# Kernel optimization log

Hardware: AMD Instinct MI355X
Metric: run time of the kernel (lower is better)

## Reference

```python
import jax, jax.numpy as jnp
import numpy as np

B, S, D, H = 4, 2048, 512, 8  # batch, seq, input_dim=feature_dim, n_heads


def setup_inputs() -> dict:
    key = jax.random.key(0)
    ks = jax.random.split(key, 12)
    s = 1.0 / np.sqrt(D)
    return {
        "q": jax.random.normal(ks[0], (B, S, D), jnp.float32),
        "k": jax.random.normal(ks[1], (B, S, D), jnp.float32),
        "v": jax.random.normal(ks[2], (B, S, D), jnp.float32),
        "mask": jax.random.randint(ks[3], (B, S), 0, 2, jnp.int32),
        "wq": jax.random.uniform(ks[4], (D, D), jnp.float32, -s, s),
        "bq": jax.random.uniform(ks[5], (D,), jnp.float32, -s, s),
        "wk": jax.random.uniform(ks[6], (D, D), jnp.float32, -s, s),
        "bk": jax.random.uniform(ks[7], (D,), jnp.float32, -s, s),
        "wv": jax.random.uniform(ks[8], (D, D), jnp.float32, -s, s),
        "bv": jax.random.uniform(ks[9], (D,), jnp.float32, -s, s),
        "wd": jax.random.uniform(ks[10], (D, D), jnp.float32, -s, s),
        "bd": jax.random.uniform(ks[11], (D,), jnp.float32, -s, s),
    }


def reference(q, k, v, mask, wq, bq, wk, bk, wv, bv, wd, bd):
    hd = D // H
    # linear projections [B,S,D]
    qp = q @ wq + bq
    kp = k @ wk + bk
    vp = v @ wv + bv
    # split heads -> [B,H,S,hd]
    split = lambda x: x.reshape(B, S, H, hd).transpose(0, 2, 1, 3)
    qh, kh, vh = split(qp), split(kp), split(vp)
    # scaled dot-product attention with additive mask [B,1,1,S]
    scores = jnp.einsum("bhqd,bhkd->bhqk", qh, kh) / np.sqrt(hd)
    scores = scores + mask.astype(scores.dtype)[:, None, None, :] * (-1e9)
    weights = jax.nn.softmax(scores, axis=-1)
    attn = jnp.einsum("bhqk,bhkd->bhqd", weights, vh)
    # merge heads -> [B,S,D], final dense
    attn = attn.transpose(0, 2, 1, 3).reshape(B, S, D)
    return attn @ wd + bd
```

## Files before the change

### kernel.cpp

```cpp
#include <hip/hip_runtime.h>
#include <hip/hip_bf16.h>
#include <cmath>

typedef __bf16 bf16;
typedef __attribute__((ext_vector_type(8))) __bf16 bf16x8;
typedef __attribute__((ext_vector_type(4))) __bf16 bf16x4;
typedef __attribute__((ext_vector_type(4))) float f32x4;
typedef __attribute__((ext_vector_type(16))) float f32x16;

#define LOG2E 1.4426950408889634f

__global__ __launch_bounds__(256)
void mask_kernel(const int* __restrict__ mask, float* __restrict__ madd)
{
    const int gid = blockIdx.x * 256 + threadIdx.x;
    madd[gid] = mask[gid] ? -1.4426950e9f : 0.f;
}

__global__ __launch_bounds__(256)
void prep_w(const float* __restrict__ w0, const float* __restrict__ w1,
            const float* __restrict__ w2, const float* __restrict__ w3,
            bf16* __restrict__ wt)
{
    const float* W = (blockIdx.z == 0) ? w0 : (blockIdx.z == 1) ? w1
                   : (blockIdx.z == 2) ? w2 : w3;
    bf16* WT = wt + (size_t)blockIdx.z * 512 * 512;

    __shared__ bf16 t[64][72];
    const int k0 = blockIdx.x * 64, n0 = blockIdx.y * 64;
    const int tid = threadIdx.x;
    {
        const int row = tid >> 2;
        const int c0 = (tid & 3) * 16;
        const float* src = W + (size_t)(k0 + row) * 512 + n0 + c0;
#pragma unroll
        for (int i = 0; i < 16; i += 4) {
            f32x4 f = *(const f32x4*)(src + i);
            t[c0 + i + 0][row] = (bf16)f[0];
            t[c0 + i + 1][row] = (bf16)f[1];
            t[c0 + i + 2][row] = (bf16)f[2];
            t[c0 + i + 3][row] = (bf16)f[3];
        }
    }
    __syncthreads();
    {
        const int nrow = tid >> 2;
        const int c0 = (tid & 3) * 16;
        bf16* dst = WT + (size_t)(n0 + nrow) * 512 + k0 + c0;
        *(bf16x8*)(dst)     = *(const bf16x8*)&t[nrow][c0];
        *(bf16x8*)(dst + 8) = *(const bf16x8*)&t[nrow][c0 + 8];
    }
}

__global__ __launch_bounds__(256)
void proj_kernel(const float* __restrict__ qin, const float* __restrict__ kin,
                 const float* __restrict__ vin, const bf16* __restrict__ wt,
                 const float* __restrict__ bq, const float* __restrict__ bk,
                 const float* __restrict__ bv, bf16* __restrict__ qp,
                 bf16* __restrict__ kf, bf16* __restrict__ vf)
{
    const int z = blockIdx.z;
    const float* A    = (z == 0) ? qin : (z == 1) ? kin : vin;
    const bf16* WT    = wt + (size_t)z * 262144;
    const float* bias = (z == 0) ? bq : (z == 1) ? bk : bv;
    const float scale = (z == 0) ? 0.125f * LOG2E : 1.0f;

    const int row0 = blockIdx.x * 64;
    const int col0 = blockIdx.y * 128;
    const int tid = threadIdx.x;
    const int wave = tid >> 6, lane = tid & 63;
    const int wr = wave >> 1, wc = wave & 1;
    const int g = lane >> 4, r = lane & 15;

    __shared__ bf16 As[64][72];
    __shared__ bf16 Bs[128][72];

    const int arow = tid >> 2, ak0 = (tid & 3) * 16;
    const int brow = tid >> 1, bk0 = (tid & 1) * 32;

    f32x4 a0, a1, a2, a3;
    bf16x8 b0, b1, b2, b3;
    {
        const float* asrc = A + (size_t)(row0 + arow) * 512 + ak0;
        a0 = *(const f32x4*)(asrc);     a1 = *(const f32x4*)(asrc + 4);
        a2 = *(const f32x4*)(asrc + 8); a3 = *(const f32x4*)(asrc + 12);
        const bf16* bsrc = WT + (size_t)(col0 + brow) * 512 + bk0;
        b0 = *(const bf16x8*)(bsrc);      b1 = *(const bf16x8*)(bsrc + 8);
        b2 = *(const bf16x8*)(bsrc + 16); b3 = *(const bf16x8*)(bsrc + 24);
    }

    f32x4 acc[2][4] = {};

    for (int kt = 0; kt < 512; kt += 64) {
        {
            bf16x8 v0, v1;
#pragma unroll
            for (int i = 0; i < 4; i++) {
                v0[i] = (bf16)a0[i]; v0[4+i] = (bf16)a1[i];
                v1[i] = (bf16)a2[i]; v1[4+i] = (bf16)a3[i];
            }
            *(bf16x8*)&As[arow][ak0]     = v0;
            *(bf16x8*)&As[arow][ak0 + 8] = v1;
            *(bf16x8*)&Bs[brow][bk0]      = b0;
            *(bf16x8*)&Bs[brow][bk0 +  8] = b1;
            *(bf16x8*)&Bs[brow][bk0 + 16] = b2;
            *(bf16x8*)&Bs[brow][bk0 + 24] = b3;
        }
        __syncthreads();

        if (kt + 64 < 512) {
            const float* asrc = A + (size_t)(row0 + arow) * 512 + kt + 64 + ak0;
            a0 = *(const f32x4*)(asrc);     a1 = *(const f32x4*)(asrc + 4);
            a2 = *(const f32x4*)(asrc + 8); a3 = *(const f32x4*)(asrc + 12);
            const bf16* bsrc = WT + (size_t)(col0 + brow) * 512 + kt + 64 + bk0;
            b0 = *(const bf16x8*)(bsrc);      b1 = *(const bf16x8*)(bsrc + 8);
            b2 = *(const bf16x8*)(bsrc + 16); b3 = *(const bf16x8*)(bsrc + 24);
        }

#pragma unroll
        for (int kk = 0; kk < 64; kk += 32) {
            bf16x8 af[2], bfr[4];
#pragma unroll
            for (int mf = 0; mf < 2; mf++)
                af[mf] = *(const bf16x8*)&As[wr*32 + mf*16 + r][kk + g*8];
#pragma unroll
            for (int nf = 0; nf < 4; nf++)
                bfr[nf] = *(const bf16x8*)&Bs[wc*64 + nf*16 + r][kk + g*8];
#pragma unroll
            for (int mf = 0; mf < 2; mf++)
#pragma unroll
                for (int nf = 0; nf < 4; nf++)
                    acc[mf][nf] = __builtin_amdgcn_mfma_f32_16x16x32_bf16(
                        af[mf], bfr[nf], acc[mf][nf], 0, 0, 0);
        }
        __syncthreads();
    }

#pragma unroll
    for (int mf = 0; mf < 2; mf++) {
#pragma unroll
        for (int nf = 0; nf < 4; nf++) {
            const int rbase = row0 + wr*32 + mf*16 + g*4;
            const int ccol  = col0 + wc*64 + nf*16 + r;
            const float bi = bias[ccol];
            const int h = ccol >> 6, hd = ccol & 63;
            if (z == 0) {
#pragma unroll
                for (int j = 0; j < 4; j++) {
                    const int rrow = rbase + j;
                    const int bb = rrow >> 11, s = rrow & 2047;
                    qp[(((size_t)(bb*8 + h) * 2048) + s) * 64 + hd] =
                        (bf16)((acc[mf][nf][j] + bi) * scale);
                }
            } else if (z == 1) {
                const int kstep = hd >> 4, khi = (hd >> 3) & 1, e = hd & 7;
#pragma unroll
                for (int j = 0; j < 4; j++) {
                    const int rrow = rbase + j;
                    const int bb = rrow >> 11, skey = rrow & 2047;
                    const int T = skey >> 6, kg = (skey >> 5) & 1, cc = skey & 31;
                    kf[(size_t)(bb*8 + h) * 131072 + T*4096 + kstep*1024
                       + kg*512 + khi*256 + cc*8 + e] = (bf16)(acc[mf][nf][j] + bi);
                }
            } else {
                const int vg = hd >> 5, cc = hd & 31;
                const int rrow = rbase;
                const int bb = rrow >> 11, skey = rrow & 2047;
                const int T = skey >> 6, kq = (skey >> 4) & 3;
                const int vhi = (skey >> 3) & 1, e0 = skey & 7;
                bf16x4 pk;
#pragma unroll
                for (int j = 0; j < 4; j++) pk[j] = (bf16)(acc[mf][nf][j] + bi);
                *(bf16x4*)&vf[(size_t)(bb*8 + h) * 131072 + T*4096 + kq*1024
                              + vg*512 + vhi*256 + cc*8 + e0] = pk;
            }
        }
    }
}

__global__ __launch_bounds__(256)
void dense_kernel(const bf16* __restrict__ ab, const bf16* __restrict__ WT,
                  const float* __restrict__ bias, float* __restrict__ out)
{
    const int row0 = blockIdx.x * 64;
    const int col0 = blockIdx.y * 128;
    const int tid = threadIdx.x;
    const int wave = tid >> 6, lane = tid & 63;
    const int wr = wave >> 1, wc = wave & 1;
    const int g = lane >> 4, r = lane & 15;

    __shared__ bf16 As[64][72];
    __shared__ bf16 Bs[128][72];

    const int arow = tid >> 2, ak0 = (tid & 3) * 16;
    const int brow = tid >> 1, bk0 = (tid & 1) * 32;

    bf16x8 aR0, aR1, b0, b1, b2, b3;
    {
        const bf16* asrc = ab + (size_t)(row0 + arow) * 512 + ak0;
        aR0 = *(const bf16x8*)(asrc); aR1 = *(const bf16x8*)(asrc + 8);
        const bf16* bsrc = WT + (size_t)(col0 + brow) * 512 + bk0;
        b0 = *(const bf16x8*)(bsrc);      b1 = *(const bf16x8*)(bsrc + 8);
        b2 = *(const bf16x8*)(bsrc + 16); b3 = *(const bf16x8*)(bsrc + 24);
    }

    f32x4 acc[2][4] = {};

    for (int kt = 0; kt < 512; kt += 64) {
        *(bf16x8*)&As[arow][ak0]     = aR0;
        *(bf16x8*)&As[arow][ak0 + 8] = aR1;
        *(bf16x8*)&Bs[brow][bk0]      = b0;
        *(bf16x8*)&Bs[brow][bk0 +  8] = b1;
        *(bf16x8*)&Bs[brow][bk0 + 16] = b2;
        *(bf16x8*)&Bs[brow][bk0 + 24] = b3;
        __syncthreads();

        if (kt + 64 < 512) {
            const bf16* asrc = ab + (size_t)(row0 + arow) * 512 + kt + 64 + ak0;
            aR0 = *(const bf16x8*)(asrc); aR1 = *(const bf16x8*)(asrc + 8);
            const bf16* bsrc = WT + (size_t)(col0 + brow) * 512 + kt + 64 + bk0;
            b0 = *(const bf16x8*)(bsrc);      b1 = *(const bf16x8*)(bsrc + 8);
            b2 = *(const bf16x8*)(bsrc + 16); b3 = *(const bf16x8*)(bsrc + 24);
        }

#pragma unroll
        for (int kk = 0; kk < 64; kk += 32) {
            bf16x8 af[2], bfr[4];
#pragma unroll
            for (int mf = 0; mf < 2; mf++)
                af[mf] = *(const bf16x8*)&As[wr*32 + mf*16 + r][kk + g*8];
#pragma unroll
            for (int nf = 0; nf < 4; nf++)
                bfr[nf] = *(const bf16x8*)&Bs[wc*64 + nf*16 + r][kk + g*8];
#pragma unroll
            for (int mf = 0; mf < 2; mf++)
#pragma unroll
                for (int nf = 0; nf < 4; nf++)
                    acc[mf][nf] = __builtin_amdgcn_mfma_f32_16x16x32_bf16(
                        af[mf], bfr[nf], acc[mf][nf], 0, 0, 0);
        }
        __syncthreads();
    }

#pragma unroll
    for (int mf = 0; mf < 2; mf++) {
#pragma unroll
        for (int nf = 0; nf < 4; nf++) {
            const int rbase = row0 + wr*32 + mf*16 + g*4;
            const int ccol  = col0 + wc*64 + nf*16 + r;
            const float bi = bias[ccol];
#pragma unroll
            for (int j = 0; j < 4; j++)
                out[(size_t)(rbase + j) * 512 + ccol] = acc[mf][nf][j] + bi;
        }
    }
}

__global__ __launch_bounds__(256)
void attn_kernel(const bf16* __restrict__ qp, const bf16* __restrict__ kf,
                 const bf16* __restrict__ vf, const float* __restrict__ madd,
                 bf16* __restrict__ attn)
{
    const int i = blockIdx.x;
    const int swz = (i & 7) * 64 + (i >> 3);
    const int bh = swz >> 4;
    const int qt = swz & 15;
    const int b = bh >> 3, h = bh & 7;
    const int tid = threadIdx.x;
    const int w = tid >> 6, lane = tid & 63;
    const int c = lane & 31;
    const int hi = lane >> 5;

    const bf16* kth = kf + (size_t)(b*8 + h) * 131072;
    const bf16* vth = vf + (size_t)(b*8 + h) * 131072;
    const float* mrow = madd + b * 2048;
    const int loff = hi*256 + c*8;
    const int q0 = qt * 128;

    bf16x8 qf[4];
    {
        const bf16* qsrc = qp + (size_t)(b*8 + h) * 2048 * 64
                         + (size_t)(q0 + w*32 + c) * 64 + hi*8;
#pragma unroll
        for (int kstep = 0; kstep < 4; kstep++)
            qf[kstep] = *(const bf16x8*)(qsrc + kstep*16);
    }

    float m_run = -INFINITY, l_run = 0.f;
    f32x16 oT0 = {}, oT1 = {};

    for (int T = 0; T < 32; T++) {
        const bf16* ktp = kth + T*4096;
        const bf16* vtp = vth + T*4096;

        bf16x8 kr[8], vr[8];
#pragma unroll
        for (int u = 0; u < 4; u++) {
            kr[u]   = *(const bf16x8*)(ktp + u*1024 + loff);
            kr[4+u] = *(const bf16x8*)(ktp + u*1024 + 512 + loff);
            vr[u]   = *(const bf16x8*)(vtp + u*1024 + loff);
            vr[4+u] = *(const bf16x8*)(vtp + u*1024 + 512 + loff);
        }
        f32x4 ma[8];
#pragma unroll
        for (int t = 0; t < 4; t++) {
            ma[t]   = *(const f32x4*)&mrow[T*64 +      t*8 + hi*4];
            ma[4+t] = *(const f32x4*)&mrow[T*64 + 32 + t*8 + hi*4];
        }

        f32x16 sa0 = {}, sa1 = {};
        __builtin_amdgcn_s_setprio(1);
#pragma unroll
        for (int kstep = 0; kstep < 4; kstep++) {
            sa0 = __builtin_amdgcn_mfma_f32_32x32x16_bf16(kr[kstep],   qf[kstep], sa0, 0, 0, 0);
            sa1 = __builtin_amdgcn_mfma_f32_32x32x16_bf16(kr[4+kstep], qf[kstep], sa1, 0, 0, 0);
        }
        __builtin_amdgcn_s_setprio(0);

#pragma unroll
        for (int t = 0; t < 4; t++) {
#pragma unroll
            for (int j = 0; j < 4; j++) {
                sa0[t*4+j] += ma[t][j];
                sa1[t*4+j] += ma[4+t][j];
            }
        }
        f32x4 vm;
#pragma unroll
        for (int j = 0; j < 4; j++)
            vm[j] = fmaxf(fmaxf(fmaxf(sa0[j], sa0[4+j]),
                                fmaxf(sa0[8+j], sa0[12+j])),
                          fmaxf(fmaxf(sa1[j], sa1[4+j]),
                                fmaxf(sa1[8+j], sa1[12+j])));
        const float mx = fmaxf(fmaxf(vm[0], vm[1]), fmaxf(vm[2], vm[3]));

        if (!__all(mx <= m_run + 11.54f)) {
            float mr = fmaxf(mx, __shfl_xor(mx, 32, 64));
            const float mn = fmaxf(m_run, mr);
            const float corr = __builtin_amdgcn_exp2f(m_run - mn);
            oT0 *= corr; oT1 *= corr; l_run *= corr;
            m_run = mn;
        }

        f32x4 ps4 = {0.f, 0.f, 0.f, 0.f};
        unsigned int z[2][4][2];
#pragma unroll
        for (int t = 0; t < 4; t++) {
            f32x4 e0, e1;
#pragma unroll
            for (int j = 0; j < 4; j++) {
                e0[j] = __builtin_amdgcn_exp2f(sa0[t*4+j] - m_run);
                e1[j] = __builtin_amdgcn_exp2f(sa1[t*4+j] - m_run);
            }
            asm("v_cvt_pk_bf16_f32 %0, %1, %2" : "=v"(z[0][t][0]) : "v"(e0[0]), "v"(e0[1]));
            asm("v_cvt_pk_bf16_f32 %0, %1, %2" : "=v"(z[0][t][1]) : "v"(e0[2]), "v"(e0[3]));
            asm("v_cvt_pk_bf16_f32 %0, %1, %2" : "=v"(z[1][t][0]) : "v"(e1[0]), "v"(e1[1]));
            asm("v_cvt_pk_bf16_f32 %0, %1, %2" : "=v"(z[1][t][1]) : "v"(e1[2]), "v"(e1[3]));
            ps4 += e0 + e1;
        }
        float psum = (ps4[0] + ps4[1]) + (ps4[2] + ps4[3]);
        psum += __shfl_xor(psum, 32, 64);
        l_run += psum;

        __builtin_amdgcn_s_setprio(1);
#pragma unroll
        for (int kg = 0; kg < 2; kg++) {
#pragma unroll
            for (int ksl = 0; ksl < 2; ksl++) {
                unsigned int a0 = z[kg][2*ksl][0], a1 = z[kg][2*ksl][1];
                unsigned int b0 = z[kg][2*ksl+1][0], b1 = z[kg][2*ksl+1][1];
                asm volatile("v_permlane32_swap_b32 %0, %1" : "+v"(a0), "+v"(b0));
                asm volatile("v_permlane32_swap_b32 %0, %1" : "+v"(a1), "+v"(b1));
                union { unsigned int u[4]; bf16x8 v; } pf;
                pf.u[0] = a0; pf.u[1] = a1; pf.u[2] = b0; pf.u[3] = b1;
                const int kq = kg*2 + ksl;
                oT0 = __builtin_amdgcn_mfma_f32_32x32x16_bf16(vr[kq],   pf.v, oT0, 0, 0, 0);
                oT1 = __builtin_amdgcn_mfma_f32_32x32x16_bf16(vr[4+kq], pf.v, oT1, 0, 0, 0);
            }
        }
        __builtin_amdgcn_s_setprio(0);
    }

    const float inv = 1.0f / l_run;
    const int s = q0 + w*32 + c;
    bf16* dst = attn + ((size_t)(b*2048) + s) * 512 + h*64;
#pragma unroll
    for (int t = 0; t < 4; t++) {
        bf16x4 o0, o1;
#pragma unroll
        for (int j = 0; j < 4; j++) {
            o0[j] = (bf16)(oT0[t*4+j] * inv);
            o1[j] = (bf16)(oT1[t*4+j] * inv);
        }
        *(bf16x4*)(dst +      t*8 + hi*4) = o0;
        *(bf16x4*)(dst + 32 + t*8 + hi*4) = o1;
    }
}

extern "C" void kernel_launch(void* const* d_in, const int* in_sizes, int n_in,
                              void* d_out, int out_size, void* d_ws, size_t ws_size,
                              hipStream_t stream)
{
    const float* q    = (const float*)d_in[0];
    const float* k    = (const float*)d_in[1];
    const float* v    = (const float*)d_in[2];
    const int*   mask = (const int*)  d_in[3];
    const float* wq   = (const float*)d_in[4];
    const float* bq   = (const float*)d_in[5];
    const float* wk   = (const float*)d_in[6];
    const float* bk   = (const float*)d_in[7];
    const float* wv   = (const float*)d_in[8];
    const float* bv   = (const float*)d_in[9];
    const float* wd   = (const float*)d_in[10];
    const float* bd   = (const float*)d_in[11];
    float* out = (float*)d_out;

    const size_t NELEM = (size_t)4 * 2048 * 512;
    bf16* qp  = (bf16*)d_ws;
    bf16* kfr = qp + NELEM;
    bf16* vfr = kfr + NELEM;
    bf16* ab  = vfr + NELEM;
    bf16* wt  = ab + NELEM;
    float* madd = (float*)(wt + 4 * 262144);

    mask_kernel<<<dim3(32), dim3(256), 0, stream>>>(mask, madd);

    prep_w<<<dim3(8, 8, 4), dim3(256), 0, stream>>>(wq, wk, wv, wd, wt);

    proj_kernel<<<dim3(128, 4, 3), dim3(256), 0, stream>>>(
        q, k, v, wt, bq, bk, bv, qp, kfr, vfr);

    attn_kernel<<<dim3(512), dim3(256), 0, stream>>>(qp, kfr, vfr, madd, ab);

    dense_kernel<<<dim3(128, 4), dim3(256), 0, stream>>>(
        ab, wt + 3*262144, bd, out);
}
```

Measured before the change: 116.1 us.

## Software-pipeline attention loop: overlap next QK MFMA with current softmax/PV

Restructures the flash-attention inner loop into a two-stage software pipeline with double-buffered score accumulators, so the QK^T MFMAs for tile T+1 are issued while softmax and PV run for tile T. K and V loads are staggered to prefetch one tile ahead. The mask add is folded into the MFMA accumulator initialisation, and exp/convert/permlane/PV are interleaved per k-slice. The cost is higher register pressure from the extra live score accumulators, which may reduce occupancy or cause spills.

```diff
diff --git a/kernel.cpp b/kernel.cpp
--- a/kernel.cpp
+++ b/kernel.cpp
@@ -288,98 +288,114 @@
 
     float m_run = -INFINITY, l_run = 0.f;
     f32x16 oT0 = {}, oT1 = {};
-
-    for (int T = 0; T < 32; T++) {
-        const bf16* ktp = kth + T*4096;
-        const bf16* vtp = vth + T*4096;
-
-        bf16x8 kr[8], vr[8];
-#pragma unroll
-        for (int u = 0; u < 4; u++) {
-            kr[u]   = *(const bf16x8*)(ktp + u*1024 + loff);
-            kr[4+u] = *(const bf16x8*)(ktp + u*1024 + 512 + loff);
-            vr[u]   = *(const bf16x8*)(vtp + u*1024 + loff);
-            vr[4+u] = *(const bf16x8*)(vtp + u*1024 + 512 + loff);
-        }
-        f32x4 ma[8];
-#pragma unroll
-        for (int t = 0; t < 4; t++) {
-            ma[t]   = *(const f32x4*)&mrow[T*64 +      t*8 + hi*4];
-            ma[4+t] = *(const f32x4*)&mrow[T*64 + 32 + t*8 + hi*4];
-        }
-
-        f32x16 sa0 = {}, sa1 = {};
-        __builtin_amdgcn_s_setprio(1);
-#pragma unroll
-        for (int kstep = 0; kstep < 4; kstep++) {
-            sa0 = __builtin_amdgcn_mfma_f32_32x32x16_bf16(kr[kstep],   qf[kstep], sa0, 0, 0, 0);
-            sa1 = __builtin_amdgcn_mfma_f32_32x32x16_bf16(kr[4+kstep], qf[kstep], sa1, 0, 0, 0);
-        }
-        __builtin_amdgcn_s_setprio(0);
-
-#pragma unroll
-        for (int t = 0; t < 4; t++) {
-#pragma unroll
-            for (int j = 0; j < 4; j++) {
-                sa0[t*4+j] += ma[t][j];
-                sa1[t*4+j] += ma[4+t][j];
-            }
-        }
-        f32x4 vm;
-#pragma unroll
-        for (int j = 0; j < 4; j++)
-            vm[j] = fmaxf(fmaxf(fmaxf(sa0[j], sa0[4+j]),
-                                fmaxf(sa0[8+j], sa0[12+j])),
-                          fmaxf(fmaxf(sa1[j], sa1[4+j]),
-                                fmaxf(sa1[8+j], sa1[12+j])));
-        const float mx = fmaxf(fmaxf(vm[0], vm[1]), fmaxf(vm[2], vm[3]));
-
-        if (!__all(mx <= m_run + 11.54f)) {
-            float mr = fmaxf(mx, __shfl_xor(mx, 32, 64));
-            const float mn = fmaxf(m_run, mr);
-            const float corr = __builtin_amdgcn_exp2f(m_run - mn);
-            oT0 *= corr; oT1 *= corr; l_run *= corr;
-            m_run = mn;
-        }
-
-        f32x4 ps4 = {0.f, 0.f, 0.f, 0.f};
-        unsigned int z[2][4][2];
-#pragma unroll
-        for (int t = 0; t < 4; t++) {
-            f32x4 e0, e1;
-#pragma unroll
-            for (int j = 0; j < 4; j++) {
-                e0[j] = __builtin_amdgcn_exp2f(sa0[t*4+j] - m_run);
-                e1[j] = __builtin_amdgcn_exp2f(sa1[t*4+j] - m_run);
-            }
-            asm("v_cvt_pk_bf16_f32 %0, %1, %2" : "=v"(z[0][t][0]) : "v"(e0[0]), "v"(e0[1]));
-            asm("v_cvt_pk_bf16_f32 %0, %1, %2" : "=v"(z[0][t][1]) : "v"(e0[2]), "v"(e0[3]));
-            asm("v_cvt_pk_bf16_f32 %0, %1, %2" : "=v"(z[1][t][0]) : "v"(e1[0]), "v"(e1[1]));
-            asm("v_cvt_pk_bf16_f32 %0, %1, %2" : "=v"(z[1][t][1]) : "v"(e1[2]), "v"(e1[3]));
-            ps4 += e0 + e1;
-        }
-        float psum = (ps4[0] + ps4[1]) + (ps4[2] + ps4[3]);
-        psum += __shfl_xor(psum, 32, 64);
-        l_run += psum;
-
-        __builtin_amdgcn_s_setprio(1);
-#pragma unroll
-        for (int kg = 0; kg < 2; kg++) {
-#pragma unroll
-            for (int ksl = 0; ksl < 2; ksl++) {
-                unsigned int a0 = z[kg][2*ksl][0], a1 = z[kg][2*ksl][1];
-                unsigned int b0 = z[kg][2*ksl+1][0], b1 = z[kg][2*ksl+1][1];
-                asm volatile("v_permlane32_swap_b32 %0, %1" : "+v"(a0), "+v"(b0));
-                asm volatile("v_permlane32_swap_b32 %0, %1" : "+v"(a1), "+v"(b1));
-                union { unsigned int u[4]; bf16x8 v; } pf;
-                pf.u[0] = a0; pf.u[1] = a1; pf.u[2] = b0; pf.u[3] = b1;
-                const int kq = kg*2 + ksl;
-                oT0 = __builtin_amdgcn_mfma_f32_32x32x16_bf16(vr[kq],   pf.v, oT0, 0, 0, 0);
-                oT1 = __builtin_amdgcn_mfma_f32_32x32x16_bf16(vr[4+kq], pf.v, oT1, 0, 0, 0);
-            }
-        }
-        __builtin_amdgcn_s_setprio(0);
-    }
+    bf16x8 kr[8], vr[8];
+    f32x16 saA0, saA1, saB0, saB1;
+
+#define LOADK(t)                                                              \
+    {   const bf16* p_ = kth + (t)*4096;                                      \
+        _Pragma("unroll")                                                     \
+        for (int u = 0; u < 4; u++) {                                         \
+            kr[u]   = *(const bf16x8*)(p_ + u*1024 + loff);                   \
+            kr[4+u] = *(const bf16x8*)(p_ + u*1024 + 512 + loff);             \
+        } }
+
+#define LOADV(t)                                                              \
+    {   const bf16* p_ = vth + (t)*4096;                                      \
+        _Pragma("unroll")                                                     \
+        for (int u = 0; u < 4; u++) {                                         \
+            vr[u]   = *(const bf16x8*)(p_ + u*1024 + loff);                   \
+            vr[4+u] = *(const bf16x8*)(p_ + u*1024 + 512 + loff);             \
+        } }
+
+#define QK_ISSUE(t, s0, s1)                                                   \
+    {   union { f32x16 v; f32x4 q[4]; } u0_, u1_;                             \
+        _Pragma("unroll")                                                     \
+        for (int tt = 0; tt < 4; tt++) {                                      \
+            u0_.q[tt] = *(const f32x4*)&mrow[(t)*64 +      tt*8 + hi*4];      \
+            u1_.q[tt] = *(const f32x4*)&mrow[(t)*64 + 32 + tt*8 + hi*4];      \
+        }                                                                     \
+        s0 = u0_.v; s1 = u1_.v;                                               \
+        __builtin_amdgcn_s_setprio(1);                                        \
+        _Pragma("unroll")                                                     \
+        for (int ks = 0; ks < 4; ks++) {                                      \
+            s0 = __builtin_amdgcn_mfma_f32_32x32x16_bf16(kr[ks],   qf[ks], s0, 0, 0, 0); \
+            s1 = __builtin_amdgcn_mfma_f32_32x32x16_bf16(kr[4+ks], qf[ks], s1, 0, 0, 0); \
+        }                                                                     \
+        __builtin_amdgcn_s_setprio(0);                                        \
+    }
+
+#define SMPV(s0, s1)                                                          \
+    {   f32x4 vm_;                                                            \
+        _Pragma("unroll")                                                     \
+        for (int j = 0; j < 4; j++)                                           \
+            vm_[j] = fmaxf(fmaxf(fmaxf(s0[j], s0[4+j]),                       \
+                                 fmaxf(s0[8+j], s0[12+j])),                   \
+                           fmaxf(fmaxf(s1[j], s1[4+j]),                       \
+                                 fmaxf(s1[8+j], s1[12+j])));                  \
+        const float mx_ = fmaxf(fmaxf(vm_[0], vm_[1]), fmaxf(vm_[2], vm_[3]));\
+        if (!__all(mx_ <= m_run + 11.54f)) {                                  \
+            float mr_ = fmaxf(mx_, __shfl_xor(mx_, 32, 64));                  \
+            const float mn_ = fmaxf(m_run, mr_);                              \
+            const float corr_ = __builtin_amdgcn_exp2f(m_run - mn_);          \
+            oT0 *= corr_; oT1 *= corr_; l_run *= corr_;                       \
+            m_run = mn_;                                                      \
+        }                                                                     \
+        f32x4 ps4_ = {0.f, 0.f, 0.f, 0.f};                                    \
+        __builtin_amdgcn_s_setprio(1);                                        \
+        _Pragma("unroll")                                                     \
+        for (int kg = 0; kg < 2; kg++) {                                      \
+            _Pragma("unroll")                                                 \
+            for (int ksl = 0; ksl < 2; ksl++) {                               \
+                f32x4 e0_, e1_;                                               \
+                _Pragma("unroll")                                             \
+                for (int j = 0; j < 4; j++) {                                 \
+                    e0_[j] = __builtin_amdgcn_exp2f(                          \
+                        (kg ? s1[(2*ksl)*4+j]   : s0[(2*ksl)*4+j])   - m_run);\
+                    e1_[j] = __builtin_amdgcn_exp2f(                          \
+                        (kg ? s1[(2*ksl+1)*4+j] : s0[(2*ksl+1)*4+j]) - m_run);\
+                }                                                             \
+                unsigned int za0_, za1_, zb0_, zb1_;                          \
+                asm("v_cvt_pk_bf16_f32 %0, %1, %2" : "=v"(za0_) : "v"(e0_[0]), "v"(e0_[1])); \
+                asm("v_cvt_pk_bf16_f32 %0, %1, %2" : "=v"(za1_) : "v"(e0_[2]), "v"(e0_[3])); \
+                asm("v_cvt_pk_bf16_f32 %0, %1, %2" : "=v"(zb0_) : "v"(e1_[0]), "v"(e1_[1])); \
+                asm("v_cvt_pk_bf16_f32 %0, %1, %2" : "=v"(zb1_) : "v"(e1_[2]), "v"(e1_[3])); \
+                asm volatile("v_permlane32_swap_b32 %0, %1" : "+v"(za0_), "+v"(zb0_)); \
+                asm volatile("v_permlane32_swap_b32 %0, %1" : "+v"(za1_), "+v"(zb1_)); \
+                union { unsigned int u[4]; bf16x8 v; } pf_;                   \
+                pf_.u[0] = za0_; pf_.u[1] = za1_; pf_.u[2] = zb0_; pf_.u[3] = zb1_; \
+                const int kq_ = kg*2 + ksl;                                   \
+                oT0 = __builtin_amdgcn_mfma_f32_32x32x16_bf16(vr[kq_],   pf_.v, oT0, 0, 0, 0); \
+                oT1 = __builtin_amdgcn_mfma_f32_32x32x16_bf16(vr[4+kq_], pf_.v, oT1, 0, 0, 0); \
+                ps4_ += e0_ + e1_;                                            \
+            }                                                                 \
+        }                                                                     \
+        __builtin_amdgcn_s_setprio(0);                                        \
+        float ps_ = (ps4_[0] + ps4_[1]) + (ps4_[2] + ps4_[3]);                \
+        ps_ += __shfl_xor(ps_, 32, 64);                                       \
+        l_run += ps_;                                                         \
+    }
+
+    LOADK(0); LOADV(0);
+    QK_ISSUE(0, saA0, saA1);
+    LOADK(1);
+
+    for (int T = 0; T < 32; T += 2) {
+        QK_ISSUE(T+1, saB0, saB1);
+        if (T + 2 < 32) LOADK(T+2);
+        SMPV(saA0, saA1);
+        LOADV(T+1);
+        if (T + 2 < 32) {
+            QK_ISSUE(T+2, saA0, saA1);
+            LOADK(T+3);
+        }
+        SMPV(saB0, saB1);
+        if (T + 2 < 32) LOADV(T+2);
+    }
+
+#undef LOADK
+#undef LOADV
+#undef QK_ISSUE
+#undef SMPV
 
     const float inv = 1.0f / l_run;
     const int s = q0 + w*32 + c;
```

New measurement: 135.1 us. +16.4%, slower.
